# Kernel tuning notes

Measured on AMD Instinct MI355X. Metric: run time of the kernel, lower is better.

The kernel has to match this reference:

```python
import jax, jax.numpy as jnp
import numpy as np

P_IDS = 8      # identities
K_PER = 8      # samples per identity per modality
D_FEAT = 2048  # feature dim
EPS = 1e-12    # F.normalize eps


def setup_inputs() -> dict:
    key = jax.random.key(0)
    B = P_IDS * 2 * K_PER  # 128
    inputs = jax.random.normal(key, (B, D_FEAT), dtype=jnp.float32)
    # Balanced PK sampling: each identity has K_PER samples in each modality.
    targets = jnp.repeat(jnp.arange(P_IDS, dtype=jnp.int32), 2 * K_PER)        # [B]
    subs = jnp.tile(jnp.repeat(jnp.arange(2, dtype=jnp.int32), K_PER), P_IDS)  # [B]
    n0 = (P_IDS - 1) * K_PER  # per-row count of (different identity, given modality)
    return {"inputs": inputs, "targets": targets, "subs": subs, "n0": n0}


def reference(inputs, targets, subs, n0):
    B, D = inputs.shape
    # centers[i] = mean of inputs over {j : targets[j]==targets[i] and subs[j]==subs[i]}
    same = (targets[:, None] == targets[None, :]) & (subs[:, None] == subs[None, :])
    w = same.astype(inputs.dtype)                                   # [B,B]
    centers = (w @ inputs) / jnp.sum(w, axis=1, keepdims=True)      # [B,D]

    diff_t = targets[:, None] != targets[None, :]
    mask0 = diff_t & (subs[None, :] == 0)                           # [B,B]
    mask1 = diff_t & (subs[None, :] == 1)
    # Boolean masking in index order -> stable argsort putting True first, take n0.
    idx0 = jnp.argsort(~mask0, axis=1)[:, :n0]                      # [B,n0]
    idx1 = jnp.argsort(~mask1, axis=1)[:, :n0]

    # Batched over i: vec_i = normalize(inputs - centers[i])
    vecs = inputs[None, :, :] - centers[:, None, :]                 # [B,B,D]
    nrm = jnp.linalg.norm(vecs, axis=-1, keepdims=True)
    vecs = vecs / jnp.maximum(nrm, EPS)
    ang = jnp.einsum('bid,bjd->bij', vecs, vecs)                    # [B,B,B]

    rows0 = jnp.take_along_axis(ang, idx0[:, :, None], axis=1)      # [B,n0,B]
    rows1 = jnp.take_along_axis(ang, idx1[:, :, None], axis=1)
    # per-i mean over n0*B elements, then / B  == overall mean (equal counts)
    loss = jnp.mean(jnp.abs(rows0 - rows1))
    return loss
```

## Files before the change

kernel.cpp:

```cpp
#include <hip/hip_runtime.h>
#include <math.h>

#define B      128
#define D      2048
#define NG     16
#define EPSN   1e-12f
#define SPLITK 4
#define KSL    (D / SPLITK)

__global__ __launch_bounds__(256) void k_gram(const float* __restrict__ X,
                                              float* __restrict__ S,
                                              float* __restrict__ out) {
    __shared__ float As[16][68];
    __shared__ float Bs[16][68];

    const int t  = threadIdx.x;
    const int tx = t & 15;
    const int ty = t >> 4;
    const int tt = blockIdx.x & 63;
    const int bj = (tt >> 3) * 16;
    const int bk = (tt & 7) * 16;
    const int k0 = (blockIdx.x >> 6) * KSL;

    const int lc = tx * 4;
    const float* rowA = &X[(bj + ty) * D + k0 + lc];
    const float* rowB = &X[(bk + ty) * D + k0 + lc];

    if (blockIdx.x == 0 && t == 0) out[0] = 0.f;

    float4 av = *reinterpret_cast<const float4*>(rowA);
    float4 bv = *reinterpret_cast<const float4*>(rowB);

    float acc = 0.f;
    const int NCH = KSL / 64;
    for (int c = 0; c < NCH; ++c) {
        As[ty][lc + 0] = av.x; As[ty][lc + 1] = av.y;
        As[ty][lc + 2] = av.z; As[ty][lc + 3] = av.w;
        Bs[ty][lc + 0] = bv.x; Bs[ty][lc + 1] = bv.y;
        Bs[ty][lc + 2] = bv.z; Bs[ty][lc + 3] = bv.w;
        __syncthreads();
        if (c + 1 < NCH) {
            av = *reinterpret_cast<const float4*>(rowA + (c + 1) * 64);
            bv = *reinterpret_cast<const float4*>(rowB + (c + 1) * 64);
        }
#pragma unroll
        for (int d = 0; d < 64; ++d)
            acc = fmaf(As[ty][d], Bs[tx][d], acc);
        __syncthreads();
    }
    atomicAdd(&S[(bj + ty) * B + (bk + tx)], acc);
}

__global__ __launch_bounds__(256) void k_loss(const float* __restrict__ S,
                                              float* __restrict__ out) {
    __shared__ float ut_s[B];
    __shared__ float inv_s[B];
    __shared__ float q_s;
    __shared__ float partial[4];

    const int t  = threadIdx.x;
    const int g  = blockIdx.x >> 2;
    const int sb = blockIdx.x & 3;
    const int base = (g >> 1) * 16 + (g & 1) * 8;
    const int tg = g >> 1;

    if (t < B) {
        float s = 0.f;
#pragma unroll
        for (int m = 0; m < 8; ++m) s += S[t * B + base + m];
        ut_s[t] = s * 0.125f;
    }
    __syncthreads();
    if (t == 0) {
        float s = 0.f;
#pragma unroll
        for (int m = 0; m < 8; ++m) s += ut_s[base + m];
        q_s = s * 0.125f;
    }
    __syncthreads();
    const float qg = q_s;
    if (t < B) {
        const float v = S[t * B + t] - 2.f * ut_s[t] + qg;
        const float n = sqrtf(fmaxf(v, 0.f));
        inv_s[t] = 1.f / fmaxf(n, EPSN);
    }
    __syncthreads();

    float sum = 0.f;
    for (int idx = t; idx < 14 * B; idx += 256) {
        const int r  = sb * 14 + (idx >> 7);
        const int k  = idx & 127;
        const int t2 = r >> 3;
        const int tp = t2 + (t2 >= tg ? 1 : 0);
        const int a  = tp * 16 + (r & 7);
        const int b  = a + 8;
        const float uk = ut_s[k];
        const float ga = (S[a * B + k] - ut_s[a] - uk + qg) * inv_s[a];
        const float gb = (S[b * B + k] - ut_s[b] - uk + qg) * inv_s[b];
        sum += fabsf(ga - gb) * inv_s[k];
    }
#pragma unroll
    for (int off = 32; off; off >>= 1) sum += __shfl_down(sum, off, 64);
    if ((t & 63) == 0) partial[t >> 6] = sum;
    __syncthreads();
    if (t == 0) {
        const float s = partial[0] + partial[1] + partial[2] + partial[3];
        atomicAdd(out, s * (8.f / (128.f * 56.f * 128.f)));
    }
}

extern "C" void kernel_launch(void* const* d_in, const int* in_sizes, int n_in,
                              void* d_out, int out_size, void* d_ws, size_t ws_size,
                              hipStream_t stream) {
    const float* X = (const float*)d_in[0];
    (void)in_sizes; (void)n_in; (void)out_size; (void)ws_size;

    float* S   = (float*)d_ws;
    float* out = (float*)d_out;

    hipMemsetAsync(S, 0, B * B * sizeof(float), stream);
    k_gram<<<64 * SPLITK, 256, 0, stream>>>(X, S, out);
    k_loss<<<NG * 4,      256, 0, stream>>>(S, out);
}
```

Baseline: 69.17 us.

## Move split-K reduction into the block and drop memset and atomics

The Gram kernel now handles all four K slices inside one block, with one 64-thread wavefront per slice. Each thread computes a 4x1 output micro-tile, and the partial sums are reduced through shared memory before one plain store. This removes the hipMemsetAsync launch and the global atomicAdds. The trade-off is a drop from 256 to 64 blocks, so fewer CUs are busy on the GPU, and each block now needs more shared memory.

```diff
diff --git a/kernel.cpp b/kernel.cpp
--- a/kernel.cpp
+++ b/kernel.cpp
@@ -1,54 +1,80 @@
 #include <hip/hip_runtime.h>
 #include <math.h>
 
-#define B      128
-#define D      2048
-#define NG     16
-#define EPSN   1e-12f
-#define SPLITK 4
-#define KSL    (D / SPLITK)
+#define B    128
+#define D    2048
+#define NG   16
+#define EPSN 1e-12f
 
 __global__ __launch_bounds__(256) void k_gram(const float* __restrict__ X,
                                               float* __restrict__ S,
                                               float* __restrict__ out) {
-    __shared__ float As[16][68];
-    __shared__ float Bs[16][68];
+    __shared__ float As[4][16][68];
+    __shared__ float Bs[4][16][68];
 
     const int t  = threadIdx.x;
-    const int tx = t & 15;
-    const int ty = t >> 4;
-    const int tt = blockIdx.x & 63;
-    const int bj = (tt >> 3) * 16;
-    const int bk = (tt & 7) * 16;
-    const int k0 = (blockIdx.x >> 6) * KSL;
-
-    const int lc = tx * 4;
-    const float* rowA = &X[(bj + ty) * D + k0 + lc];
-    const float* rowB = &X[(bk + ty) * D + k0 + lc];
+    const int kg = t >> 6;
+    const int l  = t & 63;
+    const int bj = (blockIdx.x >> 3) * 16;
+    const int bk = (blockIdx.x & 7) * 16;
+    const int k0 = kg * (D / 4);
 
     if (blockIdx.x == 0 && t == 0) out[0] = 0.f;
 
-    float4 av = *reinterpret_cast<const float4*>(rowA);
-    float4 bv = *reinterpret_cast<const float4*>(rowB);
+    const int lr = l >> 4;
+    const int lc = (l & 15) * 4;
+    const int cx = l & 15;
+    const int ry = l >> 4;
 
-    float acc = 0.f;
-    const int NCH = KSL / 64;
-    for (int c = 0; c < NCH; ++c) {
-        As[ty][lc + 0] = av.x; As[ty][lc + 1] = av.y;
-        As[ty][lc + 2] = av.z; As[ty][lc + 3] = av.w;
-        Bs[ty][lc + 0] = bv.x; Bs[ty][lc + 1] = bv.y;
-        Bs[ty][lc + 2] = bv.z; Bs[ty][lc + 3] = bv.w;
+    const float* pA = &X[bj * D + k0 + lc];
+    const float* pB = &X[bk * D + k0 + lc];
+
+    float4 a[4], b[4];
+#pragma unroll
+    for (int i = 0; i < 4; ++i) {
+        a[i] = *(const float4*)(pA + (i * 4 + lr) * D);
+        b[i] = *(const float4*)(pB + (i * 4 + lr) * D);
+    }
+
+    float acc0 = 0.f, acc1 = 0.f, acc2 = 0.f, acc3 = 0.f;
+
+    for (int c = 0; c < 8; ++c) {
+#pragma unroll
+        for (int i = 0; i < 4; ++i) {
+            const int r = i * 4 + lr;
+            As[kg][r][lc + 0] = a[i].x; As[kg][r][lc + 1] = a[i].y;
+            As[kg][r][lc + 2] = a[i].z; As[kg][r][lc + 3] = a[i].w;
+            Bs[kg][r][lc + 0] = b[i].x; Bs[kg][r][lc + 1] = b[i].y;
+            Bs[kg][r][lc + 2] = b[i].z; Bs[kg][r][lc + 3] = b[i].w;
+        }
         __syncthreads();
-        if (c + 1 < NCH) {
-            av = *reinterpret_cast<const float4*>(rowA + (c + 1) * 64);
-            bv = *reinterpret_cast<const float4*>(rowB + (c + 1) * 64);
+        if (c < 7) {
+#pragma unroll
+            for (int i = 0; i < 4; ++i) {
+                a[i] = *(const float4*)(pA + (i * 4 + lr) * D + (c + 1) * 64);
+                b[i] = *(const float4*)(pB + (i * 4 + lr) * D + (c + 1) * 64);
+            }
         }
 #pragma unroll
-        for (int d = 0; d < 64; ++d)
-            acc = fmaf(As[ty][d], Bs[tx][d], acc);
+        for (int d = 0; d < 64; ++d) {
+            const float bv = Bs[kg][cx][d];
+            acc0 = fmaf(As[kg][ry +  0][d], bv, acc0);
+            acc1 = fmaf(As[kg][ry +  4][d], bv, acc1);
+            acc2 = fmaf(As[kg][ry +  8][d], bv, acc2);
+            acc3 = fmaf(As[kg][ry + 12][d], bv, acc3);
+        }
         __syncthreads();
     }
-    atomicAdd(&S[(bj + ty) * B + (bk + tx)], acc);
+
+    Bs[kg][ry +  0][cx] = acc0;
+    Bs[kg][ry +  4][cx] = acc1;
+    Bs[kg][ry +  8][cx] = acc2;
+    Bs[kg][ry + 12][cx] = acc3;
+    __syncthreads();
+    const int row = t >> 4, col = t & 15;
+    const float s = Bs[0][row][col] + Bs[1][row][col]
+                  + Bs[2][row][col] + Bs[3][row][col];
+    S[(bj + row) * B + (bk + col)] = s;
 }
 
 __global__ __launch_bounds__(256) void k_loss(const float* __restrict__ S,
@@ -118,7 +144,6 @@
     float* S   = (float*)d_ws;
     float* out = (float*)d_out;
 
-    hipMemsetAsync(S, 0, B * B * sizeof(float), stream);
-    k_gram<<<64 * SPLITK, 256, 0, stream>>>(X, S, out);
-    k_loss<<<NG * 4,      256, 0, stream>>>(S, out);
+    k_gram<<<64,     256, 0, stream>>>(X, S, out);
+    k_loss<<<NG * 4, 256, 0, stream>>>(S, out);
 }
```

Result: slower. 82.67 us (+19.5%).
